# Kernel tuning notes

Hardware: AMD Instinct MI355X
Metric: run time of the kernel (lower is better)

The kernel has to match this reference:

```python
import jax, jax.numpy as jnp
import numpy as np

NUM_HEADS = 16
Q_HEAD_DIM = 128
KV_HEAD_DIM = 128
ROPE_DIM = 64
LATENT_DIM = 512
INPUT_DIM = 2048


def setup_inputs() -> dict:
    key = jax.random.key(0)
    ks = jax.random.split(key, 7)
    B, S, D = 2, 2048, INPUT_DIM
    x = jax.random.normal(ks[0], (B, S, D), dtype=jnp.float32)
    positions = jnp.arange(S, dtype=jnp.int32)
    # weights stored as (in, out); torch Linear computes x @ W.T with W:(out,in)
    sc = lambda fan_in: 1.0 / np.sqrt(fan_in)
    Wq = jax.random.normal(ks[1], (D, NUM_HEADS * Q_HEAD_DIM), dtype=jnp.float32) * sc(D)
    Wc = jax.random.normal(ks[2], (D, LATENT_DIM), dtype=jnp.float32) * sc(D)
    Wk = jax.random.normal(ks[3], (LATENT_DIM, NUM_HEADS * KV_HEAD_DIM), dtype=jnp.float32) * sc(LATENT_DIM)
    Wv = jax.random.normal(ks[4], (LATENT_DIM, NUM_HEADS * KV_HEAD_DIM), dtype=jnp.float32) * sc(LATENT_DIM)
    Wo = jax.random.normal(ks[5], (NUM_HEADS * KV_HEAD_DIM, D), dtype=jnp.float32) * sc(NUM_HEADS * KV_HEAD_DIM)
    return {"x": x, "positions": positions, "Wq": Wq, "Wc": Wc, "Wk": Wk, "Wv": Wv, "Wo": Wo}


def _apply_rope_q(q, positions):
    # partial RoPE on first ROPE_DIM dims of q: (B,S,H,Dq)
    half = ROPE_DIM // 2
    inv_freq = 1.0 / (10000.0 ** (jnp.arange(0, ROPE_DIM, 2, dtype=jnp.float32) / ROPE_DIM))
    freqs = positions.astype(jnp.float32)[:, None] * inv_freq[None, :]  # (S, half)
    cos = jnp.cos(freqs)[None, :, None, :]  # (1,S,1,half)
    sin = jnp.sin(freqs)[None, :, None, :]
    x1 = q[..., :half]
    x2 = q[..., half:ROPE_DIM]
    rotated = jnp.concatenate([x1 * cos - x2 * sin, x1 * sin + x2 * cos], axis=-1)
    return jnp.concatenate([rotated, q[..., ROPE_DIM:]], axis=-1)


def reference(x, positions, Wq, Wc, Wk, Wv, Wo):
    B, S, _ = x.shape
    H, Dq, Dk = NUM_HEADS, Q_HEAD_DIM, KV_HEAD_DIM
    q = (x @ Wq).reshape(B, S, H, Dq)
    kv_latent = x @ Wc                       # (B,S,latent) low-rank compression
    k = (kv_latent @ Wk).reshape(B, S, H, Dk)
    v = (kv_latent @ Wv).reshape(B, S, H, Dk)
    q = _apply_rope_q(q, positions)          # RoPE applied to q only (as in source)
    scale = 1.0 / jnp.sqrt(jnp.float32(Dq))
    scores = jnp.einsum("bqhd,bkhd->bhqk", q, k) * scale
    attn = jax.nn.softmax(scores, axis=-1)
    out = jnp.einsum("bhqk,bkhd->bqhd", attn, v).reshape(B, S, H * Dk)
    return out @ Wo
```

## Files before the change

### kernel.cpp

```cpp
#include <hip/hip_runtime.h>
#include <math.h>


typedef __attribute__((ext_vector_type(8))) short bf16x8;
typedef __attribute__((ext_vector_type(4))) float f32x4;
typedef __attribute__((ext_vector_type(16))) float f32x16;

#define GLDS(gp, lp)                                                         \
  __builtin_amdgcn_global_load_lds(                                          \
      (const __attribute__((address_space(1))) void*)(gp),                   \
      (__attribute__((address_space(3))) void*)(lp), 16, 0, 0)

__device__ __forceinline__ short f2bf(float f) {
  unsigned u = __builtin_bit_cast(unsigned, f);
  u += 0x7fffu + ((u >> 16) & 1u);
  return (short)(u >> 16);
}
__device__ __forceinline__ float b2f(short x) {
  unsigned u = ((unsigned)(unsigned short)x) << 16;
  return __builtin_bit_cast(float, u);
}
__device__ __forceinline__ unsigned cvtpk(float lo, float hi) {
  unsigned r;
  asm("v_cvt_pk_bf16_f32 %0, %1, %2" : "=v"(r) : "v"(lo), "v"(hi));
  return r;
}

__global__ void cast4_kernel(const float* __restrict__ x, short* __restrict__ xb, int n4) {
  int i = blockIdx.x * blockDim.x + threadIdx.x;
  if (i < n4) {
    float4 v = ((const float4*)x)[i];
    ushort4 o;
    o.x = (unsigned short)f2bf(v.x);
    o.y = (unsigned short)f2bf(v.y);
    o.z = (unsigned short)f2bf(v.z);
    o.w = (unsigned short)f2bf(v.w);
    ((ushort4*)xb)[i] = o;
  }
}

__global__ void transpose_cast2_kernel(const float* __restrict__ W0, short* __restrict__ T0,
                                       const float* __restrict__ W1, short* __restrict__ T1,
                                       int K, int N) {
  const float* W = blockIdx.z ? W1 : W0;
  short* Wt = blockIdx.z ? T1 : T0;
  __shared__ float tile[32][33];
  int n0 = blockIdx.x * 32, k0 = blockIdx.y * 32;
  int tx = threadIdx.x & 31, ty = threadIdx.x >> 5;
#pragma unroll
  for (int i = 0; i < 4; ++i)
    tile[ty + i * 8][tx] = W[(size_t)(k0 + ty + i * 8) * N + n0 + tx];
  __syncthreads();
#pragma unroll
  for (int i = 0; i < 4; ++i)
    Wt[(size_t)(n0 + ty + i * 8) * K + k0 + tx] = f2bf(tile[tx][ty + i * 8]);
}

__global__ void rope_tab_kernel(const int* __restrict__ pos, float* __restrict__ cosT,
                                float* __restrict__ sinT) {
  int idx = blockIdx.x * 256 + threadIdx.x;
  if (idx < 2048 * 32) {
    int s = idx >> 5, i = idx & 31;
    float p = (float)pos[s];
    float freq = p * powf(10000.0f, -(float)(2 * i) / 64.0f);
    float sv, cv;
    sincosf(freq, &sv, &cv);
    cosT[idx] = cv;
    sinT[idx] = sv;
  }
}

template <int MODE>
__device__ __forceinline__ void gemm_core(const short* __restrict__ A,
                                          const short* __restrict__ Bt,
                                          void* __restrict__ Cv,
                                          int N, int K, int bm, int bn,
                                          short* sm) {
  const int tid  = threadIdx.x;
  const int lane = tid & 63;
  const int w    = tid >> 6;
  const int col  = lane & 15, g = lane >> 4;
  const int wr = w >> 1, wc = w & 1;

  f32x4 zero4 = {0.f, 0.f, 0.f, 0.f};
  f32x4 acc[4][4];
#pragma unroll
  for (int m = 0; m < 4; ++m)
#pragma unroll
    for (int n = 0; n < 4; ++n) acc[m][n] = zero4;

  const int sr = tid >> 3;
  const int sk = tid & 7;

  auto STAGE = [&](int buf, int t) {
#pragma unroll
    for (int i = 0; i < 4; ++i) {
      int r = i * 32 + sr;
      int c = (sk ^ (r & 7)) << 3;
      GLDS(A  + (size_t)(bm + r) * K + t * 64 + c,
           sm + buf * 8192 + i * 2048 + w * 512);
      GLDS(Bt + (size_t)(bn + r) * K + t * 64 + c,
           sm + 16384 + buf * 8192 + i * 2048 + w * 512);
    }
  };

  const int nt = K >> 6;
  STAGE(0, 0);
  __syncthreads();
  int buf = 0;
  for (int t = 0; t < nt; ++t) {
    if (t + 1 < nt) STAGE(buf ^ 1, t + 1);
    const short* As = sm + buf * 8192;
    const short* Bs = sm + 16384 + buf * 8192;
#pragma unroll
    for (int kk = 0; kk < 2; ++kk) {
      bf16x8 la[4], lb[4];
#pragma unroll
      for (int m = 0; m < 4; ++m) {
        int row = wr * 64 + m * 16 + col;
        la[m] = *(const bf16x8*)(As + row * 64 + (((kk * 4 + g) ^ (row & 7)) << 3));
      }
#pragma unroll
      for (int n = 0; n < 4; ++n) {
        int row = wc * 64 + n * 16 + col;
        lb[n] = *(const bf16x8*)(Bs + row * 64 + (((kk * 4 + g) ^ (row & 7)) << 3));
      }
#pragma unroll
      for (int m = 0; m < 4; ++m)
#pragma unroll
        for (int n = 0; n < 4; ++n)
          acc[m][n] = __builtin_amdgcn_mfma_f32_16x16x32_bf16(la[m], lb[n], acc[m][n], 0, 0, 0);
    }
    __syncthreads();
    buf ^= 1;
  }

  const int orow0 = bm + wr * 64;
  const int ocol0 = bn + wc * 64;
  if (MODE == 0) {
    short* C = (short*)Cv;
#pragma unroll
    for (int m = 0; m < 4; ++m)
#pragma unroll
      for (int n = 0; n < 4; ++n)
#pragma unroll
        for (int r = 0; r < 4; ++r)
          C[(size_t)(orow0 + m * 16 + g * 4 + r) * N + ocol0 + n * 16 + col] =
              f2bf(acc[m][n][r]);
  } else if (MODE == 1) {
    float* C = (float*)Cv;
#pragma unroll
    for (int m = 0; m < 4; ++m)
#pragma unroll
      for (int n = 0; n < 4; ++n)
#pragma unroll
        for (int r = 0; r < 4; ++r)
          C[(size_t)(orow0 + m * 16 + g * 4 + r) * N + ocol0 + n * 16 + col] =
              acc[m][n][r];
  } else {
    short* C = (short*)Cv;
#pragma unroll
    for (int m = 0; m < 4; ++m)
#pragma unroll
      for (int n = 0; n < 4; ++n) {
        int grow = orow0 + m * 16 + g * 4;
        int bb = grow >> 11, s = grow & 2047;
        int cn = ocol0 + n * 16 + col;
        ushort4 pk;
        pk.x = (unsigned short)f2bf(acc[m][n][0]);
        pk.y = (unsigned short)f2bf(acc[m][n][1]);
        pk.z = (unsigned short)f2bf(acc[m][n][2]);
        pk.w = (unsigned short)f2bf(acc[m][n][3]);
        *(ushort4*)(C + ((size_t)(bb * 2048 + cn)) * 2048 + s) = pk;
      }
  }
}

__global__ __launch_bounds__(256, 2) void gemm_qc(const short* __restrict__ xb,
                                                  const short* __restrict__ wqT,
                                                  const short* __restrict__ wcT,
                                                  short* __restrict__ qb,
                                                  short* __restrict__ kvb) {
  __shared__ alignas(16) short sm[32768];
  int x = blockIdx.x, y = blockIdx.y;
  if (x < 16) gemm_core<0>(xb, wqT, qb, 2048, 2048, y * 128, x * 128, sm);
  else        gemm_core<0>(xb, wcT, kvb, 512, 2048, y * 128, (x - 16) * 128, sm);
}
__global__ __launch_bounds__(256, 2) void gemm_kv(const short* __restrict__ kvb,
                                                  const short* __restrict__ wkT,
                                                  const short* __restrict__ wvT,
                                                  short* __restrict__ kb,
                                                  short* __restrict__ vtb) {
  __shared__ alignas(16) short sm[32768];
  int x = blockIdx.x, y = blockIdx.y;
  if (x < 16) gemm_core<0>(kvb, wkT, kb, 2048, 512, y * 128, x * 128, sm);
  else        gemm_core<2>(kvb, wvT, vtb, 2048, 512, y * 128, (x - 16) * 128, sm);
}
__global__ __launch_bounds__(256, 2) void gemm_wo(const short* __restrict__ obuf,
                                                  const short* __restrict__ woT,
                                                  float* __restrict__ out) {
  __shared__ alignas(16) short sm[32768];
  gemm_core<1>(obuf, woT, out, 2048, 2048, blockIdx.y * 128, blockIdx.x * 128, sm);
}

__global__ __launch_bounds__(128, 2) void attn_kernel(
    const short* __restrict__ qb, const short* __restrict__ kb,
    const short* __restrict__ vt, short* __restrict__ ob,
    const float* __restrict__ cosT, const float* __restrict__ sinT) {
  __shared__ alignas(16) short sm[16384];
  const int tid = threadIdx.x;
  const int lane = tid & 63, w = tid >> 6;
  const int ql = lane & 31, hi = lane >> 5;
  const int qt = blockIdx.x >> 5, bh = blockIdx.x & 31;
  const int b = bh >> 4, h = bh & 15;
  const int q0w = qt * 64 + w * 32;
  const int qrow = q0w + ql;

  bf16x8 qf[8];
  {
    const short* qp = qb + ((size_t)(b * 2048 + qrow)) * 2048 + h * 128;
#pragma unroll
    for (int db = 0; db < 8; ++db) qf[db] = *(const bf16x8*)(qp + db * 16 + hi * 8);
    const float* cp = cosT + qrow * 32;
    const float* sp = sinT + qrow * 32;
#pragma unroll
    for (int db = 0; db < 2; ++db)
#pragma unroll
      for (int j = 0; j < 8; ++j) {
        int i = db * 16 + hi * 8 + j;
        float x1 = b2f(qf[db][j]), x2 = b2f(qf[db + 2][j]);
        float cv = cp[i], sv = sp[i];
        qf[db][j]     = f2bf(x1 * cv - x2 * sv);
        qf[db + 2][j] = f2bf(x1 * sv + x2 * cv);
      }
  }

  f32x16 o[4];
#pragma unroll
  for (int m4 = 0; m4 < 4; ++m4)
#pragma unroll
    for (int r = 0; r < 16; ++r) o[m4][r] = 0.f;
  float mrun = -3.0e38f, lrun = 0.f;

  auto STAGE = [&](int buf, int kt) {
#pragma unroll
    for (int i = 0; i < 4; ++i) {
      int r = i * 8 + (tid >> 4);
      int cch = tid & 15;
      const short* gp = kb + ((size_t)(b * 2048 + kt * 32 + r)) * 2048 + h * 128 +
                        ((cch ^ (r & 7)) << 3);
      GLDS(gp, sm + buf * 4096 + i * 1024 + w * 512);
    }
#pragma unroll
    for (int i = 0; i < 4; ++i) {
      int rd = i * 32 + (tid >> 2);
      int cch = tid & 3;
      const short* gp = vt + ((size_t)(b * 2048 + h * 128 + rd)) * 2048 + kt * 32 +
                        ((cch ^ ((rd >> 1) & 3)) << 3);
      GLDS(gp, sm + 8192 + buf * 4096 + i * 1024 + w * 512);
    }
  };

  const float cl2 = 0.12752744590518352f;
  STAGE(0, 0);
  __syncthreads();
  int buf = 0;
  for (int kt = 0; kt < 64; ++kt) {
    if (kt + 1 < 64) STAGE(buf ^ 1, kt + 1);
    const short* Ks = sm + buf * 4096;
    const short* Vs = sm + 8192 + buf * 4096;

    f32x16 skt;
    __builtin_amdgcn_s_setprio(1);
    {
      f32x16 a;
#pragma unroll
      for (int r = 0; r < 16; ++r) a[r] = 0.f;
#pragma unroll
      for (int db = 0; db < 8; ++db) {
        bf16x8 kf = *(const bf16x8*)(Ks + ql * 128 + (((db * 2 + hi) ^ (ql & 7)) << 3));
        a = __builtin_amdgcn_mfma_f32_32x32x16_bf16(kf, qf[db], a, 0, 0, 0);
      }
#pragma unroll
      for (int r = 0; r < 16; ++r) skt[r] = a[r] * cl2;
    }
    __builtin_amdgcn_s_setprio(0);

    float t0 = fmaxf(fmaxf(skt[0], skt[4]), fmaxf(skt[8], skt[12]));
    float t1 = fmaxf(fmaxf(skt[1], skt[5]), fmaxf(skt[9], skt[13]));
    float t2 = fmaxf(fmaxf(skt[2], skt[6]), fmaxf(skt[10], skt[14]));
    float t3 = fmaxf(fmaxf(skt[3], skt[7]), fmaxf(skt[11], skt[15]));
    float tmax = fmaxf(fmaxf(t0, t1), fmaxf(t2, t3));
    tmax = fmaxf(tmax, __shfl_xor(tmax, 32));

    if (!__all(tmax <= mrun + 8.0f)) {
      float mn = fmaxf(mrun, tmax);
      float fr = __builtin_amdgcn_exp2f(mrun - mn);
      mrun = mn;
      lrun *= fr;
#pragma unroll
      for (int m4 = 0; m4 < 4; ++m4)
#pragma unroll
        for (int r = 0; r < 16; ++r) o[m4][r] *= fr;
    }
    float s0 = 0.f, s1 = 0.f, s2 = 0.f, s3 = 0.f;
#pragma unroll
    for (int r = 0; r < 16; r += 4) {
      skt[r]     = __builtin_amdgcn_exp2f(skt[r] - mrun);
      skt[r + 1] = __builtin_amdgcn_exp2f(skt[r + 1] - mrun);
      skt[r + 2] = __builtin_amdgcn_exp2f(skt[r + 2] - mrun);
      skt[r + 3] = __builtin_amdgcn_exp2f(skt[r + 3] - mrun);
      s0 += skt[r]; s1 += skt[r + 1]; s2 += skt[r + 2]; s3 += skt[r + 3];
    }
    float psum = (s0 + s1) + (s2 + s3);
    psum += __shfl_xor(psum, 32);
    lrun += psum;

    bf16x8 pf[2];
#pragma unroll
    for (int half = 0; half < 2; ++half) {
      unsigned a0 = cvtpk(skt[half * 8 + 0], skt[half * 8 + 1]);
      unsigned a1 = cvtpk(skt[half * 8 + 2], skt[half * 8 + 3]);
      unsigned b0 = cvtpk(skt[half * 8 + 4], skt[half * 8 + 5]);
      unsigned b1 = cvtpk(skt[half * 8 + 6], skt[half * 8 + 7]);
      unsigned pa0 = __shfl_xor(a0, 32), pa1 = __shfl_xor(a1, 32);
      unsigned pb0 = __shfl_xor(b0, 32), pb1 = __shfl_xor(b1, 32);
      union { unsigned u[4]; bf16x8 v; } tmp;
      tmp.u[0] = hi ? pb0 : a0;
      tmp.u[1] = hi ? pb1 : a1;
      tmp.u[2] = hi ? b0 : pa0;
      tmp.u[3] = hi ? b1 : pa1;
      pf[half] = tmp.v;
    }

    __builtin_amdgcn_s_setprio(1);
#pragma unroll
    for (int m4 = 0; m4 < 4; ++m4) {
      int rd = m4 * 32 + ql;
#pragma unroll
      for (int ks = 0; ks < 2; ++ks) {
        bf16x8 vf = *(const bf16x8*)(Vs + rd * 32 + (((ks * 2 + hi) ^ ((rd >> 1) & 3)) << 3));
        o[m4] = __builtin_amdgcn_mfma_f32_32x32x16_bf16(vf, pf[ks], o[m4], 0, 0, 0);
      }
    }
    __builtin_amdgcn_s_setprio(0);
    __syncthreads();
    buf ^= 1;
  }

  float il = 1.0f / lrun;
  short* E = sm + w * 4352;
#pragma unroll
  for (int m4 = 0; m4 < 4; ++m4)
#pragma unroll
    for (int r = 0; r < 16; r += 2) {
      int d = m4 * 32 + (r & 3) + 8 * (r >> 2) + 4 * hi;
      unsigned pk = cvtpk(o[m4][r] * il, o[m4][r + 1] * il);
      *(unsigned*)(E + ql * 136 + d) = pk;
    }
  asm volatile("s_waitcnt lgkmcnt(0)" ::: "memory");
#pragma unroll
  for (int it = 0; it < 8; ++it) {
    int row = it * 4 + (lane >> 4);
    int ch = lane & 15;
    bf16x8 v = *(const bf16x8*)(E + row * 136 + ch * 8);
    *(bf16x8*)(ob + ((size_t)(b * 2048 + q0w + row)) * 2048 + h * 128 + ch * 8) = v;
  }
}

extern "C" void kernel_launch(void* const* d_in, const int* in_sizes, int n_in,
                              void* d_out, int out_size, void* d_ws, size_t ws_size,
                              hipStream_t stream) {
  (void)in_sizes; (void)n_in; (void)out_size; (void)ws_size;
  const float* x  = (const float*)d_in[0];
  const int*   pos = (const int*)d_in[1];
  const float* Wq = (const float*)d_in[2];
  const float* Wc = (const float*)d_in[3];
  const float* Wk = (const float*)d_in[4];
  const float* Wv = (const float*)d_in[5];
  const float* Wo = (const float*)d_in[6];

  char* ws = (char*)d_ws;
  short* xb   = (short*)(ws);
  short* qb   = (short*)(ws + 16777216);
  short* kvb  = (short*)(ws + 33554432);
  short* kb   = (short*)(ws + 37748736);
  short* vtb  = (short*)(ws + 54525952);
  short* obuf = (short*)(ws + 71303168);
  short* wqT  = (short*)(ws + 88080384);
  short* wcT  = (short*)(ws + 96468992);
  short* wkT  = (short*)(ws + 98566144);
  short* wvT  = (short*)(ws + 100663296);
  short* woT  = (short*)(ws + 102760448);
  float* cosT = (float*)(ws + 111149056);
  float* sinT = (float*)(ws + 111411200);

  cast4_kernel<<<8192, 256, 0, stream>>>(x, xb, 2097152);
  transpose_cast2_kernel<<<dim3(64, 64, 2), 256, 0, stream>>>(Wq, wqT, Wo, woT, 2048, 2048);
  transpose_cast2_kernel<<<dim3(16, 64, 1), 256, 0, stream>>>(Wc, wcT, Wc, wcT, 2048, 512);
  transpose_cast2_kernel<<<dim3(64, 16, 2), 256, 0, stream>>>(Wk, wkT, Wv, wvT, 512, 2048);
  rope_tab_kernel<<<256, 256, 0, stream>>>(pos, cosT, sinT);

  gemm_qc<<<dim3(20, 32), 256, 0, stream>>>(xb, wqT, wcT, qb, kvb);
  gemm_kv<<<dim3(32, 32), 256, 0, stream>>>(kvb, wkT, wvT, kb, vtb);

  attn_kernel<<<1024, 128, 0, stream>>>(qb, kb, vtb, obuf, cosT, sinT);

  gemm_wo<<<dim3(16, 32), 256, 0, stream>>>(obuf, woT, (float*)d_out);
}
```

Before: 252.9 us.

## Split attention key range across two wave pairs and merge partial softmax

The attention block now uses 256 threads: two wave pairs each cover half of the 2048 keys for the same 64 queries, keeping separate running max and sum, and the partial results are merged through LDS at the end. Each pair loops over 32 key tiles instead of 64. V is no longer staged into LDS; its fragments are read straight from global memory inside the loop. The aim is shorter per-block loops and more resident waves to hide latency, at the cost of an extra LDS reduction and uncoalesced global V reads that may stall the MFMA loop.

```diff
diff --git a/kernel.cpp b/kernel.cpp
--- a/kernel.cpp
+++ b/kernel.cpp
@@ -203,18 +203,20 @@
   gemm_core<1>(obuf, woT, out, 2048, 2048, blockIdx.y * 128, blockIdx.x * 128, sm);
 }
 
-__global__ __launch_bounds__(128, 2) void attn_kernel(
+__global__ __launch_bounds__(256, 4) void attn_kernel(
     const short* __restrict__ qb, const short* __restrict__ kb,
     const short* __restrict__ vt, short* __restrict__ ob,
     const float* __restrict__ cosT, const float* __restrict__ sinT) {
-  __shared__ alignas(16) short sm[16384];
+  __shared__ alignas(16) short sm[16640];
   const int tid = threadIdx.x;
   const int lane = tid & 63, w = tid >> 6;
+  const int qsub = w & 1, s = w >> 1;
   const int ql = lane & 31, hi = lane >> 5;
   const int qt = blockIdx.x >> 5, bh = blockIdx.x & 31;
   const int b = bh >> 4, h = bh & 15;
-  const int q0w = qt * 64 + w * 32;
-  const int qrow = q0w + ql;
+  const int q0 = qt * 64 + qsub * 32;
+  const int qrow = q0 + ql;
+  const int koff = s * 1024;
 
   bf16x8 qf[8];
   {
@@ -243,32 +245,24 @@
   float mrun = -3.0e38f, lrun = 0.f;
 
   auto STAGE = [&](int buf, int kt) {
+    const short* Kg = kb + ((size_t)(b * 2048 + koff + kt * 32)) * 2048 + h * 128;
+    short* dst = sm + (s * 2 + buf) * 4096;
 #pragma unroll
     for (int i = 0; i < 4; ++i) {
-      int r = i * 8 + (tid >> 4);
-      int cch = tid & 15;
-      const short* gp = kb + ((size_t)(b * 2048 + kt * 32 + r)) * 2048 + h * 128 +
-                        ((cch ^ (r & 7)) << 3);
-      GLDS(gp, sm + buf * 4096 + i * 1024 + w * 512);
-    }
-#pragma unroll
-    for (int i = 0; i < 4; ++i) {
-      int rd = i * 32 + (tid >> 2);
-      int cch = tid & 3;
-      const short* gp = vt + ((size_t)(b * 2048 + h * 128 + rd)) * 2048 + kt * 32 +
-                        ((cch ^ ((rd >> 1) & 3)) << 3);
-      GLDS(gp, sm + 8192 + buf * 4096 + i * 1024 + w * 512);
+      int r = i * 8 + qsub * 4 + (lane >> 4);
+      int cch = lane & 15;
+      GLDS(Kg + (size_t)r * 2048 + ((cch ^ (r & 7)) << 3), dst + i * 1024 + qsub * 512);
     }
   };
 
   const float cl2 = 0.12752744590518352f;
+  const short* Vg = vt + ((size_t)(b * 2048 + h * 128)) * 2048 + koff;
   STAGE(0, 0);
   __syncthreads();
   int buf = 0;
-  for (int kt = 0; kt < 64; ++kt) {
-    if (kt + 1 < 64) STAGE(buf ^ 1, kt + 1);
-    const short* Ks = sm + buf * 4096;
-    const short* Vs = sm + 8192 + buf * 4096;
+  for (int kt = 0; kt < 32; ++kt) {
+    if (kt + 1 < 32) STAGE(buf ^ 1, kt + 1);
+    const short* Ks = sm + (s * 2 + buf) * 4096;
 
     f32x16 skt;
     __builtin_amdgcn_s_setprio(1);
@@ -339,7 +333,7 @@
       int rd = m4 * 32 + ql;
 #pragma unroll
       for (int ks = 0; ks < 2; ++ks) {
-        bf16x8 vf = *(const bf16x8*)(Vs + rd * 32 + (((ks * 2 + hi) ^ ((rd >> 1) & 3)) << 3));
+        bf16x8 vf = *(const bf16x8*)(Vg + (size_t)rd * 2048 + kt * 32 + ((ks * 2 + hi) << 3));
         o[m4] = __builtin_amdgcn_mfma_f32_32x32x16_bf16(vf, pf[ks], o[m4], 0, 0, 0);
       }
     }
@@ -348,8 +342,40 @@
     buf ^= 1;
   }
 
-  float il = 1.0f / lrun;
-  short* E = sm + w * 4352;
+  float* R  = (float*)sm;
+  float* ML = (float*)(sm + 16384);
+  __syncthreads();
+  if (s == 1) {
+#pragma unroll
+    for (int m4 = 0; m4 < 4; ++m4)
+#pragma unroll
+      for (int r = 0; r < 16; ++r) {
+        int d = m4 * 32 + (r & 3) + 8 * (r >> 2) + 4 * hi;
+        R[qsub * 4096 + d * 32 + ql] = o[m4][r];
+      }
+    if (hi == 0) {
+      ML[qsub * 64 + ql * 2]     = mrun;
+      ML[qsub * 64 + ql * 2 + 1] = lrun;
+    }
+  }
+  __syncthreads();
+  if (s == 1) return;
+
+  float m1 = ML[qsub * 64 + ql * 2], l1 = ML[qsub * 64 + ql * 2 + 1];
+  float mm = fmaxf(mrun, m1);
+  float f0 = __builtin_amdgcn_exp2f(mrun - mm);
+  float f1 = __builtin_amdgcn_exp2f(m1 - mm);
+  float il = 1.0f / (lrun * f0 + l1 * f1);
+#pragma unroll
+  for (int m4 = 0; m4 < 4; ++m4)
+#pragma unroll
+    for (int r = 0; r < 16; ++r) {
+      int d = m4 * 32 + (r & 3) + 8 * (r >> 2) + 4 * hi;
+      o[m4][r] = o[m4][r] * f0 + R[qsub * 4096 + d * 32 + ql] * f1;
+    }
+  asm volatile("s_waitcnt lgkmcnt(0)" ::: "memory");
+
+  short* E = sm + qsub * 8192;
 #pragma unroll
   for (int m4 = 0; m4 < 4; ++m4)
 #pragma unroll
@@ -364,7 +390,7 @@
     int row = it * 4 + (lane >> 4);
     int ch = lane & 15;
     bf16x8 v = *(const bf16x8*)(E + row * 136 + ch * 8);
-    *(bf16x8*)(ob + ((size_t)(b * 2048 + q0w + row)) * 2048 + h * 128 + ch * 8) = v;
+    *(bf16x8*)(ob + ((size_t)(b * 2048 + q0 + row)) * 2048 + h * 128 + ch * 8) = v;
   }
 }
 
@@ -404,7 +430,7 @@
   gemm_qc<<<dim3(20, 32), 256, 0, stream>>>(xb, wqT, wcT, qb, kvb);
   gemm_kv<<<dim3(32, 32), 256, 0, stream>>>(kvb, wkT, wvT, kb, vtb);
 
-  attn_kernel<<<1024, 128, 0, stream>>>(qb, kb, vtb, obuf, cosT, sinT);
+  attn_kernel<<<1024, 256, 0, stream>>>(qb, kb, vtb, obuf, cosT, sinT);
 
   gemm_wo<<<dim3(16, 32), 256, 0, stream>>>(obuf, woT, (float*)d_out);
 }
```

After: 365.3 us. 1.44x slower.
